# Performance work log

Measured on AMD Instinct MI355X. Metric: run time of the kernel, lower is better.

Reference implementation:

```python
import jax, jax.numpy as jnp
from jax import lax
import numpy as np

D_MODEL = 1024
D_STATE = 16
D_CONV = 4
EXPAND = 2
D_INNER = EXPAND * D_MODEL  # 2048
BATCH = 4
SEQLEN = 2048


def setup_inputs() -> dict:
    key = jax.random.key(0)
    ks = jax.random.split(key, 8)
    s = 0.02  # small init scale for stability
    f32 = jnp.float32
    return {
        "x": jax.random.normal(ks[0], (BATCH, SEQLEN, D_MODEL), f32),
        # Linear weights stored as (in, out); torch applies x @ W.T with W (out, in) -- same math.
        "W_in": (jax.random.normal(ks[1], (D_MODEL, 2 * D_INNER), f32) * s),
        "conv_w": (jax.random.normal(ks[2], (D_INNER, 1, D_CONV), f32) * s),  # depthwise (O, I/groups=1, K)
        "conv_b": jnp.zeros((D_INNER,), f32),
        "W_xproj": (jax.random.normal(ks[3], (D_INNER, 2 * D_STATE), f32) * s),
        "W_dt": (jax.random.normal(ks[4], (D_INNER, D_INNER), f32) * s),
        "b_dt": jnp.zeros((D_INNER,), f32),
        "A_log": jnp.log(jax.random.uniform(ks[5], (D_INNER, D_STATE), f32, 1e-4, 1.0)),
        "D_param": jnp.ones((D_INNER,), f32),
        "W_out": (jax.random.normal(ks[6], (D_INNER, D_MODEL), f32) * s),
    }


def _mamba_forward(x, W_in, conv_w, conv_b, W_xproj, W_dt, b_dt, A_log, D_param, W_out):
    Bb, L, _ = x.shape
    # in_proj and split into x-branch and gate z
    xz = x @ W_in                      # (B, L, 2*d_inner)
    xc, z = jnp.split(xz, 2, axis=-1)
    # causal depthwise conv1d: torch pads both sides by d_conv-1 then slices [:L] == left-pad only
    xt = xc.transpose(0, 2, 1)         # (B, d_inner, L)
    xconv = lax.conv_general_dilated(
        xt, conv_w, window_strides=(1,), padding=[(D_CONV - 1, 0)],
        feature_group_count=D_INNER, dimension_numbers=("NCH", "OIH", "NCH"))
    xs = jax.nn.silu(xconv.transpose(0, 2, 1) + conv_b[None, None, :])  # (B, L, d_inner)
    # SSM inputs
    delta = jax.nn.softplus(xs @ W_dt + b_dt)          # (B, L, d_inner)
    Bs, Cs = jnp.split(xs @ W_xproj, 2, axis=-1)       # each (B, L, d_state)
    A = -jnp.exp(A_log)                                 # (d_inner, d_state)

    def step(h, inp):
        dt, bv, cv, xv = inp                            # (B,d_inner),(B,d_state),(B,d_state),(B,d_inner)
        dA = 1.0 + A[None] * dt[..., None]              # Euler discretization (B, d_inner, d_state)
        dB = bv[:, None, :] * (xv * dt)[..., None]
        h = h * dA + dB
        y = jnp.einsum("bds,bs->bd", h, cv) + D_param * xv
        return h, y

    inputs = (delta.transpose(1, 0, 2), Bs.transpose(1, 0, 2),
              Cs.transpose(1, 0, 2), xs.transpose(1, 0, 2))
    h0 = jnp.zeros((Bb, D_INNER, D_STATE), x.dtype)
    _, ys = lax.scan(step, h0, inputs)                  # ys: (L, B, d_inner)
    y = ys.transpose(1, 0, 2) * jax.nn.silu(z)          # gated output
    return y @ W_out                                    # (B, L, d_model)


def reference(x, W_in, conv_w, conv_b, W_xproj, W_dt, b_dt, A_log, D_param, W_out):
    return _mamba_forward(x, W_in, conv_w, conv_b, W_xproj, W_dt, b_dt, A_log, D_param, W_out)
```

## Files before the change

kernel.cpp:

```cpp
#include <hip/hip_runtime.h>

#define AS1 __attribute__((address_space(1)))
#define AS3 __attribute__((address_space(3)))

typedef unsigned short u16;
typedef unsigned int u32;
typedef __attribute__((ext_vector_type(8))) __bf16 bf16x8;
typedef __attribute__((ext_vector_type(8))) unsigned short u16x8;
typedef __attribute__((ext_vector_type(4))) float f32x4;

#define BATCH   4
#define SEQLEN  2048
#define DMODEL  1024
#define DINNER  2048
#define DSTATE  16
#define ROWS    (BATCH * SEQLEN)

__device__ __forceinline__ u16 f2bf(float f) {
  union { float f; unsigned u; } v; v.f = f;
  unsigned u = v.u;
  return (u16)((u + 0x7fffu + ((u >> 16) & 1u)) >> 16);
}
__device__ __forceinline__ float bf2f(u16 s) {
  union { unsigned u; float f; } v; v.u = ((unsigned)s) << 16;
  return v.f;
}
__device__ __forceinline__ float bflo(u32 p) { union { unsigned u; float f; } v; v.u = p << 16; return v.f; }
__device__ __forceinline__ float bfhi(u32 p) { union { unsigned u; float f; } v; v.u = p & 0xffff0000u; return v.f; }

template<int IMM>
__device__ __forceinline__ bf16x8 dsr(unsigned addr) {
  bf16x8 r;
  asm volatile("ds_read_b128 %0, %1 offset:%2" : "=&v"(r) : "v"(addr), "i"(IMM));
  return r;
}
__device__ __forceinline__ unsigned lds_addr(const u16* p) {
  return (unsigned)(size_t)(const AS3 u16*)p;
}

__global__ void cast_f32_bf16(const float* __restrict__ in, u16* __restrict__ out, int n4) {
  int i = blockIdx.x * blockDim.x + threadIdx.x;
  if (i >= n4) return;
  float4 v = ((const float4*)in)[i];
  ushort4 o;
  o.x = f2bf(v.x); o.y = f2bf(v.y); o.z = f2bf(v.z); o.w = f2bf(v.w);
  ((ushort4*)out)[i] = o;
}

__global__ void transpose_cast(const float* __restrict__ in, u16* __restrict__ out, int R, int C) {
  __shared__ float tile[32][33];
  int x  = blockIdx.x * 32 + threadIdx.x;
  int y0 = blockIdx.y * 32;
#pragma unroll
  for (int j = 0; j < 32; j += 8)
    tile[threadIdx.y + j][threadIdx.x] = in[(size_t)(y0 + threadIdx.y + j) * C + x];
  __syncthreads();
  int xo  = blockIdx.y * 32 + threadIdx.x;
  int yo0 = blockIdx.x * 32;
#pragma unroll
  for (int j = 0; j < 32; j += 8)
    out[(size_t)(yo0 + threadIdx.y + j) * R + xo] = f2bf(tile[threadIdx.x][threadIdx.y + j]);
}

template<int EPI>
__launch_bounds__(256, 3)
__global__ void gemm128(const u16* __restrict__ A, const u16* __restrict__ Bt,
                        void* __restrict__ outp, const float* __restrict__ bias,
                        int M, int N, int K, int gnt, int rr, int cc) {
  __shared__ u16 lds[2][2][128 * 32];

  const int xcd = blockIdx.x & 7, kb = blockIdx.x >> 3;
  const int xcols = gnt / cc;
  const int bm = (xcd / xcols) * rr + kb / cc;
  const int bn = (xcd % xcols) * cc + kb % cc;

  const int tid  = threadIdx.x;
  const int wave = tid >> 6, lane = tid & 63;
  const int wm = wave >> 1, wn = wave & 1;
  const int llo = lane & 15, lhi = lane >> 4;
  const size_t bm0 = (size_t)bm * 128, bn0 = (size_t)bn * 128;
  const int NT = K >> 5;

  const u16* gA[2]; const u16* gB[2];
#pragma unroll
  for (int c = 0; c < 2; ++c) {
    int idx = c * 256 + tid;
    int row = idx >> 2, slot = idx & 3;
    gA[c] = A  + (bm0 + row) * (size_t)K + slot * 8;
    gB[c] = Bt + (bn0 + row) * (size_t)K + slot * 8;
  }

  unsigned aA[2], aB[2];
  {
    const unsigned base = lds_addr(&lds[0][0][0]);
#pragma unroll
    for (int b = 0; b < 2; ++b) {
      aA[b] = base + b * 16384u + (unsigned)(wm * 64 + llo) * 64u + lhi * 16u;
      aB[b] = base + b * 16384u + 8192u + (unsigned)(wn * 64 + llo) * 64u + lhi * 16u;
    }
  }

#define STG(t, b) do {                                                            \
    _Pragma("unroll")                                                             \
    for (int c = 0; c < 2; ++c) {                                                 \
      __builtin_amdgcn_global_load_lds((const AS1 void*)(gA[c] + ((size_t)(t) << 5)), \
          (AS3 void*)(&lds[b][0][(c * 256 + tid) * 8]), 16, 0, 0);                \
      __builtin_amdgcn_global_load_lds((const AS1 void*)(gB[c] + ((size_t)(t) << 5)), \
          (AS3 void*)(&lds[b][1][(c * 256 + tid) * 8]), 16, 0, 0);                \
    }                                                                             \
  } while (0)

  f32x4 acc[4][4] = {};

  STG(0, 0);
  __syncthreads();

  for (int t = 0; t < NT; ++t) {
    const int cur = t & 1;
    if (t + 1 < NT) STG(t + 1, cur ^ 1);
    bf16x8 af[4], bf[4];
    {
      const unsigned a = aA[cur], b = aB[cur];
      af[0] = dsr<0>(a);    af[1] = dsr<1024>(a);
      af[2] = dsr<2048>(a); af[3] = dsr<3072>(a);
      bf[0] = dsr<0>(b);    bf[1] = dsr<1024>(b);
      bf[2] = dsr<2048>(b); bf[3] = dsr<3072>(b);
    }
    asm volatile("s_waitcnt lgkmcnt(0)" ::: "memory");
    __builtin_amdgcn_sched_barrier(0);
#pragma unroll
    for (int m = 0; m < 4; ++m)
#pragma unroll
      for (int n = 0; n < 4; ++n)
        acc[m][n] = __builtin_amdgcn_mfma_f32_16x16x32_bf16(af[m], bf[n], acc[m][n], 0, 0, 0);
    __syncthreads();
  }
#undef STG

#pragma unroll
  for (int m = 0; m < 4; ++m) {
    const int rowb = (int)bm0 + wm * 64 + m * 16 + lhi * 4;
#pragma unroll
    for (int n = 0; n < 4; ++n) {
      const int col = (int)bn0 + wn * 64 + n * 16 + llo;
#pragma unroll
      for (int r = 0; r < 4; ++r) {
        float v = acc[m][n][r];
        size_t idx = (size_t)(rowb + r) * N + col;
        if (EPI == 0) {
          ((u16*)outp)[idx] = f2bf(v);
        } else if (EPI == 1) {
          float xb = v + bias[col];
          float sp = (xb > 20.f) ? xb : log1pf(__expf(xb));
          ((u16*)outp)[idx] = f2bf(sp);
        } else {
          ((float*)outp)[idx] = v;
        }
      }
    }
  }
}

__global__ void conv_silu4(const u16* __restrict__ xz, const float* __restrict__ w,
                           const float* __restrict__ cb, u16* __restrict__ xs, int total4) {
  int idx = blockIdx.x * 256 + threadIdx.x;
  if (idx >= total4) return;
  int d4 = idx & (DINNER / 4 - 1);
  int l  = (idx >> 9) & (SEQLEN - 1);
  int b  = idx >> 20;
  int d  = d4 * 4;
  float4 wv[4];
#pragma unroll
  for (int j = 0; j < 4; ++j) wv[j] = ((const float4*)w)[d + j];
  float4 bias = *(const float4*)(cb + d);
  float acc[4] = { bias.x, bias.y, bias.z, bias.w };
#pragma unroll
  for (int k = 0; k < 4; ++k) {
    int li = l - 3 + k;
    if (li >= 0) {
      ushort4 xv = *(const ushort4*)(xz + (size_t)(b * SEQLEN + li) * (2 * DINNER) + d);
      acc[0] = fmaf((&wv[0].x)[k], bf2f(xv.x), acc[0]);
      acc[1] = fmaf((&wv[1].x)[k], bf2f(xv.y), acc[1]);
      acc[2] = fmaf((&wv[2].x)[k], bf2f(xv.z), acc[2]);
      acc[3] = fmaf((&wv[3].x)[k], bf2f(xv.w), acc[3]);
    }
  }
  ushort4 o;
  o.x = f2bf(acc[0] / (1.f + __expf(-acc[0])));
  o.y = f2bf(acc[1] / (1.f + __expf(-acc[1])));
  o.z = f2bf(acc[2] / (1.f + __expf(-acc[2])));
  o.w = f2bf(acc[3] / (1.f + __expf(-acc[3])));
  *(ushort4*)(xs + (size_t)idx * 4) = o;
}

__global__ void xproj_kernel(const u16* __restrict__ xs, const float* __restrict__ Wx,
                             float* __restrict__ outp) {
  __shared__ float part[256];
  int row = blockIdx.x;
  int tid = threadIdx.x;
  int c = tid & 31, kp = tid >> 5;
  const u16* xr = xs + (size_t)row * DINNER + kp * 256;
  const float* wp = Wx + (size_t)(kp * 256) * 32 + c;
  float acc = 0.f;
#pragma unroll 4
  for (int kk = 0; kk < 32; ++kk) {
    u16x8 xv = *(const u16x8*)(const void*)(xr + kk * 8);
#pragma unroll
    for (int j = 0; j < 8; ++j)
      acc = fmaf(bf2f(xv[j]), wp[(kk * 8 + j) * 32], acc);
  }
  part[tid] = acc;
  __syncthreads();
  if (tid < 32) {
    float s = 0.f;
#pragma unroll
    for (int p = 0; p < 8; ++p) s += part[p * 32 + tid];
    outp[(size_t)row * 32 + tid] = s;
  }
}

#define SC_NC 32
#define SC_CL 64
#define SC_LDS (2 * SC_NC * 16 * 33 * 4)

__launch_bounds__(512, 1)
__global__ void scan_v3(const u16* __restrict__ delta, const u16* __restrict__ xs,
                        const float* __restrict__ xproj, const u16* __restrict__ xz,
                        const float* __restrict__ A_log, const float* __restrict__ Dp,
                        u16* __restrict__ yg) {
  extern __shared__ float smem[];
  float* cP = smem;
  float* cH = smem + SC_NC * 16 * 33;
  const int tid = threadIdx.x;
  const int dl = tid & 15, ck = tid >> 4;
  const int b = blockIdx.x >> 6, dblk = blockIdx.x & 63;
  const int d0 = dblk * 32 + dl * 2;
  const int r0 = b * SEQLEN + ck * SC_CL;

  float A0[DSTATE], A1[DSTATE];
  {
    const f32x4* ap0 = (const f32x4*)(A_log + (size_t)d0 * DSTATE);
    const f32x4* ap1 = (const f32x4*)(A_log + (size_t)(d0 + 1) * DSTATE);
#pragma unroll
    for (int q = 0; q < 4; ++q) {
      f32x4 a0 = ap0[q], a1 = ap1[q];
#pragma unroll
      for (int j = 0; j < 4; ++j) { A0[q * 4 + j] = -__expf(a0[j]); A1[q * 4 + j] = -__expf(a1[j]); }
    }
  }

  const u32* dP = (const u32*)(delta + (size_t)r0 * DINNER + d0);
  const u32* xP = (const u32*)(xs    + (size_t)r0 * DINNER + d0);
  const u32* zP = (const u32*)(xz + (size_t)r0 * (2 * DINNER) + DINNER + d0);
  const float* bP = xproj + (size_t)r0 * 32;
  const int DW = DINNER / 2;
  const int ZW = DINNER;

  float P0[DSTATE], P1[DSTATE], H0[DSTATE], H1[DSTATE];
#pragma unroll
  for (int s = 0; s < DSTATE; ++s) { P0[s] = P1[s] = 1.f; H0[s] = H1[s] = 0.f; }
  {
    u32 dq0 = dP[0], xq0 = xP[0];
    u32 dq1 = dP[DW], xq1 = xP[DW];
    f32x4 Bn[4];
#pragma unroll
    for (int q = 0; q < 4; ++q) Bn[q] = ((const f32x4*)bP)[q];
    for (int l = 0; l < SC_CL; ++l) {
      const u32 dc = dq0, xc = xq0;
      dq0 = dq1; xq0 = xq1;
      if (l + 2 < SC_CL) { dq1 = dP[(l + 2) * DW]; xq1 = xP[(l + 2) * DW]; }
      f32x4 Bc[4] = { Bn[0], Bn[1], Bn[2], Bn[3] };
      if (l + 1 < SC_CL) {
        const f32x4* bn = (const f32x4*)(bP + (l + 1) * 32);
#pragma unroll
        for (int q = 0; q < 4; ++q) Bn[q] = bn[q];
      }
      float dt0 = bflo(dc), dt1 = bfhi(dc);
      float x0 = bflo(xc),  x1 = bfhi(xc);
      float dtx0 = dt0 * x0, dtx1 = dt1 * x1;
#pragma unroll
      for (int s = 0; s < DSTATE; ++s) {
        float bs = Bc[s >> 2][s & 3];
        float dA0 = fmaf(A0[s], dt0, 1.f);
        float dA1 = fmaf(A1[s], dt1, 1.f);
        P0[s] *= dA0; P1[s] *= dA1;
        H0[s] = fmaf(H0[s], dA0, bs * dtx0);
        H1[s] = fmaf(H1[s], dA1, bs * dtx1);
      }
    }
  }
  {
    float* p = cP + (ck * 16 + dl) * 33;
    float* h = cH + (ck * 16 + dl) * 33;
#pragma unroll
    for (int s = 0; s < DSTATE; ++s) {
      p[s] = P0[s]; p[16 + s] = P1[s];
      h[s] = H0[s]; h[16 + s] = H1[s];
    }
  }
  __syncthreads();

  {
    const int s2 = tid & 15, dd = tid >> 4;
    const int idx = (dd & 1) * 16 + s2;
    float* pbase = cP + (dd >> 1) * 33 + idx;
    float* hbase = cH + (dd >> 1) * 33 + idx;
    float h = 0.f;
    for (int c = 0; c < SC_NC; ++c) {
      float p = pbase[c * 16 * 33], hh = hbase[c * 16 * 33];
      pbase[c * 16 * 33] = h;
      h = fmaf(p, h, hh);
    }
  }
  __syncthreads();

  float h0[DSTATE], h1[DSTATE];
  {
    const float* p = cP + (ck * 16 + dl) * 33;
#pragma unroll
    for (int s = 0; s < DSTATE; ++s) { h0[s] = p[s]; h1[s] = p[16 + s]; }
  }
  const float Dv0 = Dp[d0], Dv1 = Dp[d0 + 1];
  u32* yP = (u32*)(yg + (size_t)r0 * DINNER + d0);
  {
    u32 dq0 = dP[0], xq0 = xP[0], zq0 = zP[0];
    u32 dq1 = dP[DW], xq1 = xP[DW], zq1 = zP[ZW];
    f32x4 Bn[4], Cn[4];
#pragma unroll
    for (int q = 0; q < 4; ++q) { Bn[q] = ((const f32x4*)bP)[q]; Cn[q] = ((const f32x4*)bP)[q + 4]; }
    for (int l = 0; l < SC_CL; ++l) {
      const u32 dc = dq0, xc = xq0, zc = zq0;
      dq0 = dq1; xq0 = xq1; zq0 = zq1;
      if (l + 2 < SC_CL) { dq1 = dP[(l + 2) * DW]; xq1 = xP[(l + 2) * DW]; zq1 = zP[(l + 2) * ZW]; }
      f32x4 Bc[4] = { Bn[0], Bn[1], Bn[2], Bn[3] };
      f32x4 Cc[4] = { Cn[0], Cn[1], Cn[2], Cn[3] };
      if (l + 1 < SC_CL) {
        const f32x4* bn = (const f32x4*)(bP + (l + 1) * 32);
#pragma unroll
        for (int q = 0; q < 4; ++q) { Bn[q] = bn[q]; Cn[q] = bn[q + 4]; }
      }
      float dt0 = bflo(dc), dt1 = bfhi(dc);
      float x0 = bflo(xc),  x1 = bfhi(xc);
      float dtx0 = dt0 * x0, dtx1 = dt1 * x1;
      float yp0 = 0.f, yp1 = 0.f;
#pragma unroll
      for (int s = 0; s < DSTATE; ++s) {
        float bs = Bc[s >> 2][s & 3];
        float cs = Cc[s >> 2][s & 3];
        float dA0 = fmaf(A0[s], dt0, 1.f);
        float dA1 = fmaf(A1[s], dt1, 1.f);
        h0[s] = fmaf(h0[s], dA0, bs * dtx0);
        h1[s] = fmaf(h1[s], dA1, bs * dtx1);
        yp0 = fmaf(h0[s], cs, yp0);
        yp1 = fmaf(h1[s], cs, yp1);
      }
      float z0 = bflo(zc), z1 = bfhi(zc);
      float y0 = (yp0 + Dv0 * x0) * (z0 / (1.f + __expf(-z0)));
      float y1 = (yp1 + Dv1 * x1) * (z1 / (1.f + __expf(-z1)));
      yP[l * DW] = (u32)f2bf(y0) | ((u32)f2bf(y1) << 16);
    }
  }
}

extern "C" void kernel_launch(void* const* d_in, const int* in_sizes, int n_in,
                              void* d_out, int out_size, void* d_ws, size_t ws_size,
                              hipStream_t stream) {
  const float* x       = (const float*)d_in[0];
  const float* W_in    = (const float*)d_in[1];
  const float* conv_w  = (const float*)d_in[2];
  const float* conv_b  = (const float*)d_in[3];
  const float* W_xproj = (const float*)d_in[4];
  const float* W_dt    = (const float*)d_in[5];
  const float* b_dt    = (const float*)d_in[6];
  const float* A_log   = (const float*)d_in[7];
  const float* D_param = (const float*)d_in[8];
  const float* W_out   = (const float*)d_in[9];
  float* out = (float*)d_out;

  char* ws = (char*)d_ws;
  const size_t MB = 1ull << 20;
  u16*   x_bf  = (u16*)(ws);
  u16*   WinT  = (u16*)(ws + 16 * MB);
  u16*   WdtT  = (u16*)(ws + 24 * MB);
  u16*   xz_bf = (u16*)(ws + 32 * MB);
  u16*   xs_bf = (u16*)(ws + 96 * MB);
  u16*   delta = (u16*)(ws + 128 * MB);
  float* xpj   = (float*)(ws + 192 * MB);
  u16*   WoutT = (u16*)(ws + 193 * MB);
  u16*   yg    = (u16*)(ws);

  hipFuncSetAttribute((const void*)scan_v3, hipFuncAttributeMaxDynamicSharedMemorySize, SC_LDS);

  dim3 tb(32, 8);

  cast_f32_bf16<<<(ROWS * DMODEL / 4 + 255) / 256, 256, 0, stream>>>(x, x_bf, ROWS * DMODEL / 4);
  transpose_cast<<<dim3((2 * DINNER) / 32, DMODEL / 32), tb, 0, stream>>>(W_in, WinT, DMODEL, 2 * DINNER);
  transpose_cast<<<dim3(DINNER / 32, DINNER / 32), tb, 0, stream>>>(W_dt, WdtT, DINNER, DINNER);
  transpose_cast<<<dim3(DMODEL / 32, DINNER / 32), tb, 0, stream>>>(W_out, WoutT, DINNER, DMODEL);

  gemm128<0><<<2048, 256, 0, stream>>>(x_bf, WinT, xz_bf, nullptr,
                                       ROWS, 2 * DINNER, DMODEL, 32, 32, 8);

  conv_silu4<<<(ROWS * DINNER / 4) / 256, 256, 0, stream>>>(
      xz_bf, conv_w, conv_b, xs_bf, ROWS * DINNER / 4);

  gemm128<1><<<1024, 256, 0, stream>>>(xs_bf, WdtT, delta, b_dt,
                                       ROWS, DINNER, DINNER, 16, 32, 4);

  xproj_kernel<<<ROWS, 256, 0, stream>>>(xs_bf, W_xproj, xpj);

  scan_v3<<<BATCH * (DINNER / 32), 512, SC_LDS, stream>>>(
      delta, xs_bf, xpj, xz_bf, A_log, D_param, yg);

  gemm128<2><<<512, 256, 0, stream>>>(yg, WoutT, out, nullptr,
                                      ROWS, DMODEL, DINNER, 8, 16, 4);
}
```

Measured before the change: 497.2 us.

## Load GEMM B operand directly to registers, widen K-tile, swizzle A in LDS

Rewrites the bf16 GEMM main loop so the B operand is loaded from global memory straight into registers, prefetched one K-step ahead. Only A is staged through LDS, now with a 64-wide K tile and an XOR swizzle to avoid bank conflicts. The MFMA work is split into two halves with partial lgkmcnt waits so the second half's LDS reads overlap the first half's compute. This reduces LDS traffic and barrier count per K element, at the cost of more registers (launch bounds lowered to 2 blocks per SM) and uncoalesced-ish per-lane global B loads.

```diff
diff --git a/kernel.cpp b/kernel.cpp
--- a/kernel.cpp
+++ b/kernel.cpp
@@ -36,6 +36,11 @@
 }
 __device__ __forceinline__ unsigned lds_addr(const u16* p) {
   return (unsigned)(size_t)(const AS3 u16*)p;
+}
+template<int N>
+__device__ __forceinline__ void lgkm() {
+  asm volatile("s_waitcnt lgkmcnt(%0)" :: "i"(N) : "memory");
+  __builtin_amdgcn_sched_barrier(0);
 }
 
 __global__ void cast_f32_bf16(const float* __restrict__ in, u16* __restrict__ out, int n4) {
@@ -63,11 +68,11 @@
 }
 
 template<int EPI>
-__launch_bounds__(256, 3)
-__global__ void gemm128(const u16* __restrict__ A, const u16* __restrict__ Bt,
-                        void* __restrict__ outp, const float* __restrict__ bias,
-                        int M, int N, int K, int gnt, int rr, int cc) {
-  __shared__ u16 lds[2][2][128 * 32];
+__launch_bounds__(256, 2)
+__global__ void gemm128v(const u16* __restrict__ A, const u16* __restrict__ Bt,
+                         void* __restrict__ outp, const float* __restrict__ bias,
+                         int M, int N, int K, int gnt, int rr, int cc) {
+  __shared__ u16 lds[2][128 * 64];
 
   const int xcd = blockIdx.x & 7, kb = blockIdx.x >> 3;
   const int xcols = gnt / cc;
@@ -79,61 +84,84 @@
   const int wm = wave >> 1, wn = wave & 1;
   const int llo = lane & 15, lhi = lane >> 4;
   const size_t bm0 = (size_t)bm * 128, bn0 = (size_t)bn * 128;
-  const int NT = K >> 5;
-
-  const u16* gA[2]; const u16* gB[2];
-#pragma unroll
-  for (int c = 0; c < 2; ++c) {
+  const int NT = K >> 6;
+
+  const u16* gA[4];
+#pragma unroll
+  for (int c = 0; c < 4; ++c) {
     int idx = c * 256 + tid;
-    int row = idx >> 2, slot = idx & 3;
-    gA[c] = A  + (bm0 + row) * (size_t)K + slot * 8;
-    gB[c] = Bt + (bn0 + row) * (size_t)K + slot * 8;
-  }
-
-  unsigned aA[2], aB[2];
-  {
-    const unsigned base = lds_addr(&lds[0][0][0]);
-#pragma unroll
-    for (int b = 0; b < 2; ++b) {
-      aA[b] = base + b * 16384u + (unsigned)(wm * 64 + llo) * 64u + lhi * 16u;
-      aB[b] = base + b * 16384u + 8192u + (unsigned)(wn * 64 + llo) * 64u + lhi * 16u;
-    }
+    int row = idx >> 3, slot = idx & 7;
+    gA[c] = A + (bm0 + row) * (size_t)K + ((slot ^ (row & 7)) << 3);
+  }
+  const u16* gBw = Bt + (bn0 + (size_t)(wn * 64 + llo)) * K + lhi * 8;
+  const size_t nK = (size_t)16 * K;
+
+  unsigned aA[2][2];
+  {
+    const unsigned base = lds_addr(&lds[0][0]);
+#pragma unroll
+    for (int b = 0; b < 2; ++b)
+#pragma unroll
+      for (int kk = 0; kk < 2; ++kk) {
+        unsigned gran = (((unsigned)(kk * 4 + lhi)) ^ ((unsigned)llo & 7u)) << 4;
+        aA[b][kk] = base + (unsigned)b * 16384u + (unsigned)(wm * 64 + llo) * 128u + gran;
+      }
   }
 
 #define STG(t, b) do {                                                            \
     _Pragma("unroll")                                                             \
-    for (int c = 0; c < 2; ++c) {                                                 \
-      __builtin_amdgcn_global_load_lds((const AS1 void*)(gA[c] + ((size_t)(t) << 5)), \
-          (AS3 void*)(&lds[b][0][(c * 256 + tid) * 8]), 16, 0, 0);                \
-      __builtin_amdgcn_global_load_lds((const AS1 void*)(gB[c] + ((size_t)(t) << 5)), \
-          (AS3 void*)(&lds[b][1][(c * 256 + tid) * 8]), 16, 0, 0);                \
-    }                                                                             \
+    for (int c = 0; c < 4; ++c)                                                   \
+      __builtin_amdgcn_global_load_lds((const AS1 void*)(gA[c] + ((size_t)(t) << 6)), \
+          (AS3 void*)(&lds[b][(c * 256 + tid) * 8]), 16, 0, 0);                   \
   } while (0)
 
   f32x4 acc[4][4] = {};
+  bf16x8 bc0[4], bc1[4];
 
   STG(0, 0);
+#pragma unroll
+  for (int n = 0; n < 4; ++n) {
+    bc0[n] = *(const bf16x8*)(const void*)(gBw + n * nK);
+    bc1[n] = *(const bf16x8*)(const void*)(gBw + 32 + n * nK);
+  }
   __syncthreads();
 
   for (int t = 0; t < NT; ++t) {
     const int cur = t & 1;
-    if (t + 1 < NT) STG(t + 1, cur ^ 1);
-    bf16x8 af[4], bf[4];
+    bf16x8 bn0_[4], bn1_[4];
+    const bool more = (t + 1) < NT;
+    if (more) {
+      const u16* p = gBw + ((size_t)(t + 1) << 6);
+#pragma unroll
+      for (int n = 0; n < 4; ++n) {
+        bn0_[n] = *(const bf16x8*)(const void*)(p + n * nK);
+        bn1_[n] = *(const bf16x8*)(const void*)(p + 32 + n * nK);
+      }
+      STG(t + 1, cur ^ 1);
+    }
+    bf16x8 af0[4], af1[4];
     {
-      const unsigned a = aA[cur], b = aB[cur];
-      af[0] = dsr<0>(a);    af[1] = dsr<1024>(a);
-      af[2] = dsr<2048>(a); af[3] = dsr<3072>(a);
-      bf[0] = dsr<0>(b);    bf[1] = dsr<1024>(b);
-      bf[2] = dsr<2048>(b); bf[3] = dsr<3072>(b);
-    }
-    asm volatile("s_waitcnt lgkmcnt(0)" ::: "memory");
-    __builtin_amdgcn_sched_barrier(0);
+      const unsigned a0 = aA[cur][0], a1 = aA[cur][1];
+      af0[0] = dsr<0>(a0); af0[1] = dsr<2048>(a0); af0[2] = dsr<4096>(a0); af0[3] = dsr<6144>(a0);
+      af1[0] = dsr<0>(a1); af1[1] = dsr<2048>(a1); af1[2] = dsr<4096>(a1); af1[3] = dsr<6144>(a1);
+    }
+    lgkm<4>();
 #pragma unroll
     for (int m = 0; m < 4; ++m)
 #pragma unroll
       for (int n = 0; n < 4; ++n)
-        acc[m][n] = __builtin_amdgcn_mfma_f32_16x16x32_bf16(af[m], bf[n], acc[m][n], 0, 0, 0);
+        acc[m][n] = __builtin_amdgcn_mfma_f32_16x16x32_bf16(af0[m], bc0[n], acc[m][n], 0, 0, 0);
+    lgkm<0>();
+#pragma unroll
+    for (int m = 0; m < 4; ++m)
+#pragma unroll
+      for (int n = 0; n < 4; ++n)
+        acc[m][n] = __builtin_amdgcn_mfma_f32_16x16x32_bf16(af1[m], bc1[n], acc[m][n], 0, 0, 0);
     __syncthreads();
+    if (more) {
+#pragma unroll
+      for (int n = 0; n < 4; ++n) { bc0[n] = bn0_[n]; bc1[n] = bn1_[n]; }
+    }
   }
 #undef STG
 
@@ -398,20 +426,20 @@
   transpose_cast<<<dim3(DINNER / 32, DINNER / 32), tb, 0, stream>>>(W_dt, WdtT, DINNER, DINNER);
   transpose_cast<<<dim3(DMODEL / 32, DINNER / 32), tb, 0, stream>>>(W_out, WoutT, DINNER, DMODEL);
 
-  gemm128<0><<<2048, 256, 0, stream>>>(x_bf, WinT, xz_bf, nullptr,
-                                       ROWS, 2 * DINNER, DMODEL, 32, 32, 8);
+  gemm128v<0><<<2048, 256, 0, stream>>>(x_bf, WinT, xz_bf, nullptr,
+                                        ROWS, 2 * DINNER, DMODEL, 32, 32, 8);
 
   conv_silu4<<<(ROWS * DINNER / 4) / 256, 256, 0, stream>>>(
       xz_bf, conv_w, conv_b, xs_bf, ROWS * DINNER / 4);
 
-  gemm128<1><<<1024, 256, 0, stream>>>(xs_bf, WdtT, delta, b_dt,
-                                       ROWS, DINNER, DINNER, 16, 32, 4);
+  gemm128v<1><<<1024, 256, 0, stream>>>(xs_bf, WdtT, delta, b_dt,
+                                        ROWS, DINNER, DINNER, 16, 32, 4);
 
   xproj_kernel<<<ROWS, 256, 0, stream>>>(xs_bf, W_xproj, xpj);
 
   scan_v3<<<BATCH * (DINNER / 32), 512, SC_LDS, stream>>>(
       delta, xs_bf, xpj, xz_bf, A_log, D_param, yg);
 
-  gemm128<2><<<512, 256, 0, stream>>>(yg, WoutT, out, nullptr,
-                                      ROWS, DMODEL, DINNER, 8, 16, 4);
-}
+  gemm128v<2><<<512, 256, 0, stream>>>(yg, WoutT, out, nullptr,
+                                       ROWS, DMODEL, DINNER, 8, 16, 4);
+}
```

Result: slower. 646.6 us (+30.1%).

## Replace 128x128 GEMM with 256-row triple-buffered swizzled-LDS GEMM

Applied to the files above, without the earlier changes.

Swaps the 128x128, 256-thread double-buffered GEMM for a 512-thread kernel with 256xBN tiles (BN of 256 or 128) and a three-stage LDS ring fed by global_load_lds. The LDS layout is XOR-swizzled to avoid bank conflicts, and explicit vmcnt/lgkmcnt waits with raw barriers and setprio around the MFMA block replace __syncthreads. Larger tiles are meant to raise arithmetic intensity and cut global and LDS traffic per FLOP, while deeper prefetch hides load latency. The cost is one block per CU with high register and LDS use, and fewer blocks per launch, which may leave the last wave of the grid partly idle.

```diff
diff --git a/kernel.cpp b/kernel.cpp
--- a/kernel.cpp
+++ b/kernel.cpp
@@ -36,6 +36,15 @@
 }
 __device__ __forceinline__ unsigned lds_addr(const u16* p) {
   return (unsigned)(size_t)(const AS3 u16*)p;
+}
+template<int N>
+__device__ __forceinline__ void lgkm() {
+  asm volatile("s_waitcnt lgkmcnt(%0)" :: "i"(N) : "memory");
+  __builtin_amdgcn_sched_barrier(0);
+}
+template<int N>
+__device__ __forceinline__ void vmw() {
+  asm volatile("s_waitcnt vmcnt(%0)" :: "i"(N) : "memory");
 }
 
 __global__ void cast_f32_bf16(const float* __restrict__ in, u16* __restrict__ out, int n4) {
@@ -62,90 +71,118 @@
     out[(size_t)(yo0 + threadIdx.y + j) * R + xo] = f2bf(tile[threadIdx.x][threadIdx.y + j]);
 }
 
-template<int EPI>
-__launch_bounds__(256, 3)
-__global__ void gemm128(const u16* __restrict__ A, const u16* __restrict__ Bt,
+template<int EPI, int BN_>
+__launch_bounds__(512, 1)
+__global__ void gemm2ph(const u16* __restrict__ A, const u16* __restrict__ Bt,
                         void* __restrict__ outp, const float* __restrict__ bias,
-                        int M, int N, int K, int gnt, int rr, int cc) {
-  __shared__ u16 lds[2][2][128 * 32];
+                        int M, int N, int K, int gn, int rr, int cc) {
+  constexpr int NF   = BN_ / 64;
+  constexpr int ASZ  = 256 * 32;
+  constexpr int BSZ  = BN_ * 32;
+  constexpr int BUFS = ASZ + BSZ;
+  constexpr int BUFB = BUFS * 2;
+  constexpr int NLB  = BN_ / 128;
+  constexpr int L    = 2 + NLB;
+  extern __shared__ u16 lds[];
 
   const int xcd = blockIdx.x & 7, kb = blockIdx.x >> 3;
-  const int xcols = gnt / cc;
-  const int bm = (xcd / xcols) * rr + kb / cc;
-  const int bn = (xcd % xcols) * cc + kb % cc;
+  const int tpr = gn / cc;
+  const int bm  = (xcd / tpr) * rr + kb / cc;
+  const int bn  = (xcd % tpr) * cc + kb % cc;
 
   const int tid  = threadIdx.x;
   const int wave = tid >> 6, lane = tid & 63;
-  const int wm = wave >> 1, wn = wave & 1;
+  const int wm = wave >> 2, wn = wave & 3;
   const int llo = lane & 15, lhi = lane >> 4;
-  const size_t bm0 = (size_t)bm * 128, bn0 = (size_t)bn * 128;
+  const size_t bm0 = (size_t)bm * 256, bn0 = (size_t)bn * BN_;
   const int NT = K >> 5;
 
-  const u16* gA[2]; const u16* gB[2];
-#pragma unroll
-  for (int c = 0; c < 2; ++c) {
-    int idx = c * 256 + tid;
-    int row = idx >> 2, slot = idx & 3;
-    gA[c] = A  + (bm0 + row) * (size_t)K + slot * 8;
-    gB[c] = Bt + (bn0 + row) * (size_t)K + slot * 8;
-  }
-
-  unsigned aA[2], aB[2];
-  {
-    const unsigned base = lds_addr(&lds[0][0][0]);
-#pragma unroll
-    for (int b = 0; b < 2; ++b) {
-      aA[b] = base + b * 16384u + (unsigned)(wm * 64 + llo) * 64u + lhi * 16u;
-      aB[b] = base + b * 16384u + 8192u + (unsigned)(wn * 64 + llo) * 64u + lhi * 16u;
-    }
-  }
-
-#define STG(t, b) do {                                                            \
-    _Pragma("unroll")                                                             \
-    for (int c = 0; c < 2; ++c) {                                                 \
-      __builtin_amdgcn_global_load_lds((const AS1 void*)(gA[c] + ((size_t)(t) << 5)), \
-          (AS3 void*)(&lds[b][0][(c * 256 + tid) * 8]), 16, 0, 0);                \
-      __builtin_amdgcn_global_load_lds((const AS1 void*)(gB[c] + ((size_t)(t) << 5)), \
-          (AS3 void*)(&lds[b][1][(c * 256 + tid) * 8]), 16, 0, 0);                \
-    }                                                                             \
+  const int srow = tid >> 2;
+  const int fr   = ((tid >> 2) & 3) ^ ((tid >> 4) & 3);
+  const int scol = ((tid & 3) ^ fr) << 3;
+  const u16* gA[2];
+  gA[0] = A + (bm0 + srow) * (size_t)K + scol;
+  gA[1] = A + (bm0 + 128 + srow) * (size_t)K + scol;
+  const u16* gB[2];
+  gB[0] = Bt + (bn0 + srow) * (size_t)K + scol;
+  gB[1] = (NLB == 2) ? (Bt + (bn0 + 128 + srow) * (size_t)K + scol) : gB[0];
+
+  const unsigned base = lds_addr(lds);
+  const unsigned gsw  = (unsigned)((lhi ^ (llo & 3) ^ (llo >> 2)) << 4);
+  const unsigned rdA0 = base + (unsigned)(wm * 128 + llo) * 64u + gsw;
+  const unsigned rdB0 = base + (unsigned)ASZ * 2 + (unsigned)(wn * (NF * 16) + llo) * 64u + gsw;
+
+#define SG(t, stgoff) do {                                                        \
+    __builtin_amdgcn_global_load_lds((const AS1 void*)(gA[0] + ((size_t)(t) << 5)), \
+        (AS3 void*)(lds + (stgoff) + wave * 8), 16, 0, 0);                        \
+    __builtin_amdgcn_global_load_lds((const AS1 void*)(gA[1] + ((size_t)(t) << 5)), \
+        (AS3 void*)(lds + (stgoff) + 4096 + wave * 8), 16, 0, 0);                 \
+    __builtin_amdgcn_global_load_lds((const AS1 void*)(gB[0] + ((size_t)(t) << 5)), \
+        (AS3 void*)(lds + (stgoff) + ASZ + wave * 8), 16, 0, 0);                  \
+    if (NLB == 2)                                                                 \
+      __builtin_amdgcn_global_load_lds((const AS1 void*)(gB[1] + ((size_t)(t) << 5)), \
+          (AS3 void*)(lds + (stgoff) + ASZ + 4096 + wave * 8), 16, 0, 0);         \
   } while (0)
-
-  f32x4 acc[4][4] = {};
-
-  STG(0, 0);
-  __syncthreads();
+#undef SG
+#define SG(t, stgoff) do {                                                        \
+    __builtin_amdgcn_global_load_lds((const AS1 void*)(gA[0] + ((size_t)(t) << 5)), \
+        (AS3 void*)(lds + (stgoff) + wave * 512), 16, 0, 0);                      \
+    __builtin_amdgcn_global_load_lds((const AS1 void*)(gA[1] + ((size_t)(t) << 5)), \
+        (AS3 void*)(lds + (stgoff) + 4096 + wave * 512), 16, 0, 0);               \
+    __builtin_amdgcn_global_load_lds((const AS1 void*)(gB[0] + ((size_t)(t) << 5)), \
+        (AS3 void*)(lds + (stgoff) + ASZ + wave * 512), 16, 0, 0);                \
+    if (NLB == 2)                                                                 \
+      __builtin_amdgcn_global_load_lds((const AS1 void*)(gB[1] + ((size_t)(t) << 5)), \
+          (AS3 void*)(lds + (stgoff) + ASZ + 4096 + wave * 512), 16, 0, 0);       \
+  } while (0)
+
+  f32x4 acc[8][NF] = {};
+
+  SG(0, 0);
+  SG(1, BUFS);
+  vmw<L>();
+  asm volatile("s_barrier" ::: "memory");
+
+  unsigned rdA = rdA0, rdB = rdB0;
+  unsigned stg = 2 * BUFS;
 
   for (int t = 0; t < NT; ++t) {
-    const int cur = t & 1;
-    if (t + 1 < NT) STG(t + 1, cur ^ 1);
-    bf16x8 af[4], bf[4];
-    {
-      const unsigned a = aA[cur], b = aB[cur];
-      af[0] = dsr<0>(a);    af[1] = dsr<1024>(a);
-      af[2] = dsr<2048>(a); af[3] = dsr<3072>(a);
-      bf[0] = dsr<0>(b);    bf[1] = dsr<1024>(b);
-      bf[2] = dsr<2048>(b); bf[3] = dsr<3072>(b);
-    }
-    asm volatile("s_waitcnt lgkmcnt(0)" ::: "memory");
-    __builtin_amdgcn_sched_barrier(0);
-#pragma unroll
-    for (int m = 0; m < 4; ++m)
-#pragma unroll
-      for (int n = 0; n < 4; ++n)
-        acc[m][n] = __builtin_amdgcn_mfma_f32_16x16x32_bf16(af[m], bf[n], acc[m][n], 0, 0, 0);
-    __syncthreads();
-  }
-#undef STG
-
-#pragma unroll
-  for (int m = 0; m < 4; ++m) {
-    const int rowb = (int)bm0 + wm * 64 + m * 16 + lhi * 4;
-#pragma unroll
-    for (int n = 0; n < 4; ++n) {
-      const int col = (int)bn0 + wn * 64 + n * 16 + llo;
+    bf16x8 af[8], bf[4];
+    af[0] = dsr<0>(rdA);    af[1] = dsr<1024>(rdA);
+    af[2] = dsr<2048>(rdA); af[3] = dsr<3072>(rdA);
+    af[4] = dsr<4096>(rdA); af[5] = dsr<5120>(rdA);
+    af[6] = dsr<6144>(rdA); af[7] = dsr<7168>(rdA);
+    bf[0] = dsr<0>(rdB);    bf[1] = dsr<1024>(rdB);
+    if (NF == 4) { bf[2] = dsr<2048>(rdB); bf[3] = dsr<3072>(rdB); }
+    const bool st = (t + 2) < NT;
+    if (st) SG(t + 2, stg);
+    asm volatile("s_barrier" ::: "memory");
+    lgkm<0>();
+    __builtin_amdgcn_s_setprio(1);
+#pragma unroll
+    for (int am = 0; am < 8; ++am)
+#pragma unroll
+      for (int n = 0; n < NF; ++n)
+        acc[am][n] = __builtin_amdgcn_mfma_f32_16x16x32_bf16(af[am], bf[n], acc[am][n], 0, 0, 0);
+    __builtin_amdgcn_s_setprio(0);
+    if (st) vmw<L>(); else vmw<0>();
+    asm volatile("s_barrier" ::: "memory");
+    rdA += BUFB; rdB += BUFB;
+    if (rdA >= rdA0 + 3 * BUFB) { rdA -= 3 * BUFB; rdB -= 3 * BUFB; }
+    stg += BUFS; if (stg >= 3 * BUFS) stg -= 3 * BUFS;
+  }
+#undef SG
+
+#pragma unroll
+  for (int am = 0; am < 8; ++am) {
+    const int mh = am >> 2, m = am & 3;
+    const int rowb = (int)bm0 + wm * 128 + mh * 64 + m * 16 + lhi * 4;
+#pragma unroll
+    for (int n = 0; n < NF; ++n) {
+      const int col = (int)bn0 + wn * (16 * NF) + n * 16 + llo;
 #pragma unroll
       for (int r = 0; r < 4; ++r) {
-        float v = acc[m][n][r];
+        float v = acc[am][n][r];
         size_t idx = (size_t)(rowb + r) * N + col;
         if (EPI == 0) {
           ((u16*)outp)[idx] = f2bf(v);
@@ -389,6 +426,9 @@
   u16*   WoutT = (u16*)(ws + 193 * MB);
   u16*   yg    = (u16*)(ws);
 
+  hipFuncSetAttribute((const void*)gemm2ph<0, 256>, hipFuncAttributeMaxDynamicSharedMemorySize, 98304);
+  hipFuncSetAttribute((const void*)gemm2ph<1, 256>, hipFuncAttributeMaxDynamicSharedMemorySize, 98304);
+  hipFuncSetAttribute((const void*)gemm2ph<2, 128>, hipFuncAttributeMaxDynamicSharedMemorySize, 73728);
   hipFuncSetAttribute((const void*)scan_v3, hipFuncAttributeMaxDynamicSharedMemorySize, SC_LDS);
 
   dim3 tb(32, 8);
@@ -398,20 +438,20 @@
   transpose_cast<<<dim3(DINNER / 32, DINNER / 32), tb, 0, stream>>>(W_dt, WdtT, DINNER, DINNER);
   transpose_cast<<<dim3(DMODEL / 32, DINNER / 32), tb, 0, stream>>>(W_out, WoutT, DINNER, DMODEL);
 
-  gemm128<0><<<2048, 256, 0, stream>>>(x_bf, WinT, xz_bf, nullptr,
-                                       ROWS, 2 * DINNER, DMODEL, 32, 32, 8);
+  gemm2ph<0, 256><<<512, 512, 98304, stream>>>(x_bf, WinT, xz_bf, nullptr,
+                                               ROWS, 2 * DINNER, DMODEL, 16, 8, 8);
 
   conv_silu4<<<(ROWS * DINNER / 4) / 256, 256, 0, stream>>>(
       xz_bf, conv_w, conv_b, xs_bf, ROWS * DINNER / 4);
 
-  gemm128<1><<<1024, 256, 0, stream>>>(xs_bf, WdtT, delta, b_dt,
-                                       ROWS, DINNER, DINNER, 16, 32, 4);
+  gemm2ph<1, 256><<<256, 512, 98304, stream>>>(xs_bf, WdtT, delta, b_dt,
+                                               ROWS, DINNER, DINNER, 8, 4, 8);
 
   xproj_kernel<<<ROWS, 256, 0, stream>>>(xs_bf, W_xproj, xpj);
 
   scan_v3<<<BATCH * (DINNER / 32), 512, SC_LDS, stream>>>(
       delta, xs_bf, xpj, xz_bf, A_log, D_param, yg);
 
-  gemm128<2><<<512, 256, 0, stream>>>(yg, WoutT, out, nullptr,
-                                      ROWS, DMODEL, DINNER, 8, 16, 4);
-}
+  gemm2ph<2, 128><<<256, 512, 73728, stream>>>(yg, WoutT, out, nullptr,
+                                               ROWS, DMODEL, DINNER, 8, 4, 8);
+}
```

Measured after the change: 496.3 us. No clear change (-0.2%).

## Restructure bf16 GEMM to 8 waves, BK=64 with XOR-swizzled LDS

Applied to the files above, without the earlier changes.

Replaces the 256-thread GEMM with a 512-thread version (2x4 waves, each computing 64x32) that stages 64-wide K tiles into dynamic LDS using an XOR swizzle to avoid bank conflicts. The K loop is split into two 32-wide halves, with explicit barriers, waitcnts and s_setprio around the MFMA blocks. The aim is to halve loop iterations, reduce LDS conflicts and improve latency hiding for the three projection GEMMs. In exchange it uses 64KB of LDS per block, which limits occupancy, and relies on hand-placed barriers whose correctness and timing are delicate.

```diff
diff --git a/kernel.cpp b/kernel.cpp
--- a/kernel.cpp
+++ b/kernel.cpp
@@ -36,6 +36,15 @@
 }
 __device__ __forceinline__ unsigned lds_addr(const u16* p) {
   return (unsigned)(size_t)(const AS3 u16*)p;
+}
+template<int N>
+__device__ __forceinline__ void lgkm() {
+  asm volatile("s_waitcnt lgkmcnt(%0)" :: "i"(N) : "memory");
+  __builtin_amdgcn_sched_barrier(0);
+}
+template<int N>
+__device__ __forceinline__ void vmw() {
+  asm volatile("s_waitcnt vmcnt(%0)" :: "i"(N) : "memory");
 }
 
 __global__ void cast_f32_bf16(const float* __restrict__ in, u16* __restrict__ out, int n4) {
@@ -63,86 +72,113 @@
 }
 
 template<int EPI>
-__launch_bounds__(256, 3)
-__global__ void gemm128(const u16* __restrict__ A, const u16* __restrict__ Bt,
-                        void* __restrict__ outp, const float* __restrict__ bias,
-                        int M, int N, int K, int gnt, int rr, int cc) {
-  __shared__ u16 lds[2][2][128 * 32];
+__launch_bounds__(512, 4)
+__global__ void gemm128d(const u16* __restrict__ A, const u16* __restrict__ Bt,
+                         void* __restrict__ outp, const float* __restrict__ bias,
+                         int M, int N, int K, int gn, int rr, int cc) {
+  constexpr int ASZ  = 128 * 64;
+  constexpr int BUFS = 2 * ASZ;
+  extern __shared__ u16 lds[];
 
   const int xcd = blockIdx.x & 7, kb = blockIdx.x >> 3;
-  const int xcols = gnt / cc;
-  const int bm = (xcd / xcols) * rr + kb / cc;
-  const int bn = (xcd % xcols) * cc + kb % cc;
+  const int tpr = gn / cc;
+  const int bm  = (xcd / tpr) * rr + kb / cc;
+  const int bn  = (xcd % tpr) * cc + kb % cc;
 
   const int tid  = threadIdx.x;
   const int wave = tid >> 6, lane = tid & 63;
-  const int wm = wave >> 1, wn = wave & 1;
+  const int wm = wave >> 2, wn = wave & 3;
   const int llo = lane & 15, lhi = lane >> 4;
   const size_t bm0 = (size_t)bm * 128, bn0 = (size_t)bn * 128;
-  const int NT = K >> 5;
-
+  const int NT = K >> 6;
+
+  const int srow = tid >> 3;
+  const int scol = ((tid & 7) ^ (srow & 7)) << 3;
   const u16* gA[2]; const u16* gB[2];
-#pragma unroll
-  for (int c = 0; c < 2; ++c) {
-    int idx = c * 256 + tid;
-    int row = idx >> 2, slot = idx & 3;
-    gA[c] = A  + (bm0 + row) * (size_t)K + slot * 8;
-    gB[c] = Bt + (bn0 + row) * (size_t)K + slot * 8;
-  }
-
-  unsigned aA[2], aB[2];
-  {
-    const unsigned base = lds_addr(&lds[0][0][0]);
-#pragma unroll
-    for (int b = 0; b < 2; ++b) {
-      aA[b] = base + b * 16384u + (unsigned)(wm * 64 + llo) * 64u + lhi * 16u;
-      aB[b] = base + b * 16384u + 8192u + (unsigned)(wn * 64 + llo) * 64u + lhi * 16u;
-    }
-  }
-
-#define STG(t, b) do {                                                            \
-    _Pragma("unroll")                                                             \
-    for (int c = 0; c < 2; ++c) {                                                 \
-      __builtin_amdgcn_global_load_lds((const AS1 void*)(gA[c] + ((size_t)(t) << 5)), \
-          (AS3 void*)(&lds[b][0][(c * 256 + tid) * 8]), 16, 0, 0);                \
-      __builtin_amdgcn_global_load_lds((const AS1 void*)(gB[c] + ((size_t)(t) << 5)), \
-          (AS3 void*)(&lds[b][1][(c * 256 + tid) * 8]), 16, 0, 0);                \
-    }                                                                             \
+  gA[0] = A  + (bm0 + srow) * (size_t)K + scol;
+  gA[1] = A  + (bm0 + 64 + srow) * (size_t)K + scol;
+  gB[0] = Bt + (bn0 + srow) * (size_t)K + scol;
+  gB[1] = Bt + (bn0 + 64 + srow) * (size_t)K + scol;
+
+  unsigned aA[2][2], aB[2][2];
+  {
+    const unsigned base0 = lds_addr(lds);
+    const unsigned rowA = (unsigned)(wm * 64 + llo) * 128u;
+    const unsigned rowB = (unsigned)(wn * 32 + llo) * 128u;
+    const unsigned msk = (unsigned)((llo & 7) << 4);
+#pragma unroll
+    for (int bf = 0; bf < 2; ++bf)
+#pragma unroll
+      for (int kk = 0; kk < 2; ++kk) {
+        unsigned colk = ((unsigned)(kk * 64 + lhi * 16)) ^ msk;
+        aA[bf][kk] = base0 + (unsigned)bf * (BUFS * 2) + rowA + colk;
+        aB[bf][kk] = base0 + (unsigned)bf * (BUFS * 2) + (ASZ * 2) + rowB + colk;
+      }
+  }
+
+#define SG(t, bsel) do {                                                          \
+    __builtin_amdgcn_global_load_lds((const AS1 void*)(gA[0] + ((size_t)(t) << 6)), \
+        (AS3 void*)(lds + (bsel) * BUFS + wave * 512), 16, 0, 0);                 \
+    __builtin_amdgcn_global_load_lds((const AS1 void*)(gA[1] + ((size_t)(t) << 6)), \
+        (AS3 void*)(lds + (bsel) * BUFS + 4096 + wave * 512), 16, 0, 0);          \
+    __builtin_amdgcn_global_load_lds((const AS1 void*)(gB[0] + ((size_t)(t) << 6)), \
+        (AS3 void*)(lds + (bsel) * BUFS + ASZ + wave * 512), 16, 0, 0);           \
+    __builtin_amdgcn_global_load_lds((const AS1 void*)(gB[1] + ((size_t)(t) << 6)), \
+        (AS3 void*)(lds + (bsel) * BUFS + ASZ + 4096 + wave * 512), 16, 0, 0);    \
   } while (0)
 
-  f32x4 acc[4][4] = {};
-
-  STG(0, 0);
-  __syncthreads();
+  f32x4 acc[4][2] = {};
+
+  SG(0, 0);
+  vmw<0>();
+  asm volatile("s_barrier" ::: "memory");
 
   for (int t = 0; t < NT; ++t) {
     const int cur = t & 1;
-    if (t + 1 < NT) STG(t + 1, cur ^ 1);
-    bf16x8 af[4], bf[4];
+    const bool more = (t + 1) < NT;
+    if (more) SG(t + 1, cur ^ 1);
     {
-      const unsigned a = aA[cur], b = aB[cur];
-      af[0] = dsr<0>(a);    af[1] = dsr<1024>(a);
-      af[2] = dsr<2048>(a); af[3] = dsr<3072>(a);
-      bf[0] = dsr<0>(b);    bf[1] = dsr<1024>(b);
-      bf[2] = dsr<2048>(b); bf[3] = dsr<3072>(b);
-    }
-    asm volatile("s_waitcnt lgkmcnt(0)" ::: "memory");
-    __builtin_amdgcn_sched_barrier(0);
-#pragma unroll
-    for (int m = 0; m < 4; ++m)
-#pragma unroll
-      for (int n = 0; n < 4; ++n)
-        acc[m][n] = __builtin_amdgcn_mfma_f32_16x16x32_bf16(af[m], bf[n], acc[m][n], 0, 0, 0);
-    __syncthreads();
-  }
-#undef STG
+      bf16x8 af[4], bf[2];
+      af[0] = dsr<0>(aA[cur][0]);    af[1] = dsr<2048>(aA[cur][0]);
+      af[2] = dsr<4096>(aA[cur][0]); af[3] = dsr<6144>(aA[cur][0]);
+      bf[0] = dsr<0>(aB[cur][0]);    bf[1] = dsr<2048>(aB[cur][0]);
+      asm volatile("s_barrier" ::: "memory");
+      lgkm<0>();
+      __builtin_amdgcn_s_setprio(1);
+#pragma unroll
+      for (int m = 0; m < 4; ++m)
+#pragma unroll
+        for (int n = 0; n < 2; ++n)
+          acc[m][n] = __builtin_amdgcn_mfma_f32_16x16x32_bf16(af[m], bf[n], acc[m][n], 0, 0, 0);
+      __builtin_amdgcn_s_setprio(0);
+      asm volatile("s_barrier" ::: "memory");
+    }
+    {
+      bf16x8 af[4], bf[2];
+      af[0] = dsr<0>(aA[cur][1]);    af[1] = dsr<2048>(aA[cur][1]);
+      af[2] = dsr<4096>(aA[cur][1]); af[3] = dsr<6144>(aA[cur][1]);
+      bf[0] = dsr<0>(aB[cur][1]);    bf[1] = dsr<2048>(aB[cur][1]);
+      asm volatile("s_barrier" ::: "memory");
+      lgkm<0>();
+      __builtin_amdgcn_s_setprio(1);
+#pragma unroll
+      for (int m = 0; m < 4; ++m)
+#pragma unroll
+        for (int n = 0; n < 2; ++n)
+          acc[m][n] = __builtin_amdgcn_mfma_f32_16x16x32_bf16(af[m], bf[n], acc[m][n], 0, 0, 0);
+      __builtin_amdgcn_s_setprio(0);
+      vmw<0>();
+      asm volatile("s_barrier" ::: "memory");
+    }
+  }
+#undef SG
 
 #pragma unroll
   for (int m = 0; m < 4; ++m) {
     const int rowb = (int)bm0 + wm * 64 + m * 16 + lhi * 4;
 #pragma unroll
-    for (int n = 0; n < 4; ++n) {
-      const int col = (int)bn0 + wn * 64 + n * 16 + llo;
+    for (int n = 0; n < 2; ++n) {
+      const int col = (int)bn0 + wn * 32 + n * 16 + llo;
 #pragma unroll
       for (int r = 0; r < 4; ++r) {
         float v = acc[m][n][r];
@@ -389,6 +425,9 @@
   u16*   WoutT = (u16*)(ws + 193 * MB);
   u16*   yg    = (u16*)(ws);
 
+  hipFuncSetAttribute((const void*)gemm128d<0>, hipFuncAttributeMaxDynamicSharedMemorySize, 65536);
+  hipFuncSetAttribute((const void*)gemm128d<1>, hipFuncAttributeMaxDynamicSharedMemorySize, 65536);
+  hipFuncSetAttribute((const void*)gemm128d<2>, hipFuncAttributeMaxDynamicSharedMemorySize, 65536);
   hipFuncSetAttribute((const void*)scan_v3, hipFuncAttributeMaxDynamicSharedMemorySize, SC_LDS);
 
   dim3 tb(32, 8);
@@ -398,20 +437,20 @@
   transpose_cast<<<dim3(DINNER / 32, DINNER / 32), tb, 0, stream>>>(W_dt, WdtT, DINNER, DINNER);
   transpose_cast<<<dim3(DMODEL / 32, DINNER / 32), tb, 0, stream>>>(W_out, WoutT, DINNER, DMODEL);
 
-  gemm128<0><<<2048, 256, 0, stream>>>(x_bf, WinT, xz_bf, nullptr,
-                                       ROWS, 2 * DINNER, DMODEL, 32, 32, 8);
+  gemm128d<0><<<2048, 512, 65536, stream>>>(x_bf, WinT, xz_bf, nullptr,
+                                            ROWS, 2 * DINNER, DMODEL, 32, 32, 8);
 
   conv_silu4<<<(ROWS * DINNER / 4) / 256, 256, 0, stream>>>(
       xz_bf, conv_w, conv_b, xs_bf, ROWS * DINNER / 4);
 
-  gemm128<1><<<1024, 256, 0, stream>>>(xs_bf, WdtT, delta, b_dt,
-                                       ROWS, DINNER, DINNER, 16, 32, 4);
+  gemm128d<1><<<1024, 512, 65536, stream>>>(xs_bf, WdtT, delta, b_dt,
+                                            ROWS, DINNER, DINNER, 16, 32, 4);
 
   xproj_kernel<<<ROWS, 256, 0, stream>>>(xs_bf, W_xproj, xpj);
 
   scan_v3<<<BATCH * (DINNER / 32), 512, SC_LDS, stream>>>(
       delta, xs_bf, xpj, xz_bf, A_log, D_param, yg);
 
-  gemm128<2><<<512, 256, 0, stream>>>(yg, WoutT, out, nullptr,
-                                      ROWS, DMODEL, DINNER, 8, 16, 4);
-}
+  gemm128d<2><<<512, 512, 65536, stream>>>(yg, WoutT, out, nullptr,
+                                           ROWS, DMODEL, DINNER, 8, 16, 4);
+}
```

After: 480.1 us. 3.4% less time.
